# Kernel optimization log

Hardware: AMD Instinct MI355X
Metric: run time of the kernel (lower is better)

## Reference

```python
import jax, jax.numpy as jnp
import numpy as np

D = 192      # d_model
DE = 96      # d_edge
H = 8        # n_heads
DH = D // H  # d_head = 24
DF = 2 * D   # ff hidden = 384
N = 25000
E = 400000


def _layernorm(x, s, b, eps=1e-5):
    m = jnp.mean(x, axis=-1, keepdims=True)
    v = jnp.var(x, axis=-1, keepdims=True)
    return (x - m) * jax.lax.rsqrt(v + eps) * s + b


def setup_inputs() -> dict:
    key = jax.random.key(0)
    ks = jax.random.split(key, 12)
    sc = lambda d: 1.0 / np.sqrt(d)
    inp = {
        "x": jax.random.normal(ks[0], (N, D), jnp.float32),
        "edge_feat": jax.random.normal(ks[1], (E, DE), jnp.float32),
        "edge_index": jax.random.randint(ks[2], (2, E), 0, N, jnp.int64),
        # attention projections (stored [d_in, d_out], applied as x @ W)
        "Wq": jax.random.normal(ks[3], (D, D), jnp.float32) * sc(D),
        "Wk": jax.random.normal(ks[4], (D, D), jnp.float32) * sc(D),
        "Wv": jax.random.normal(ks[5], (D, D), jnp.float32) * sc(D),
        "We": jax.random.normal(ks[6], (DE, H), jnp.float32) * sc(DE),
        "Wo": jax.random.normal(ks[7], (D, D), jnp.float32) * sc(D),
        "bo": jnp.zeros((D,), jnp.float32),
        "Wg": jax.random.normal(ks[8], (2 * D, D), jnp.float32) * sc(2 * D),
        "bg": jnp.zeros((D,), jnp.float32),
        "ln1_s": jnp.ones((D,), jnp.float32),
        "ln1_b": jnp.zeros((D,), jnp.float32),
        "Wf1": jax.random.normal(ks[9], (D, DF), jnp.float32) * sc(D),
        "bf1": jnp.zeros((DF,), jnp.float32),
        "Wf2": jax.random.normal(ks[10], (DF, D), jnp.float32) * sc(DF),
        "bf2": jnp.zeros((D,), jnp.float32),
        "ln2_s": jnp.ones((D,), jnp.float32),
        "ln2_b": jnp.zeros((D,), jnp.float32),
    }
    return inp


def reference(x, edge_feat, edge_index, Wq, Wk, Wv, We, Wo, bo, Wg, bg,
              ln1_s, ln1_b, Wf1, bf1, Wf2, bf2, ln2_s, ln2_b):
    src, dst = edge_index[0], edge_index[1]
    n = x.shape[0]
    # per-edge gathered projections: [E, H, DH]
    q = (x[dst] @ Wq).reshape(-1, H, DH)
    k = (x[src] @ Wk).reshape(-1, H, DH)
    v = (x[src] @ Wv).reshape(-1, H, DH)
    score = jnp.sum(q * k, axis=-1) / np.sqrt(DH) + edge_feat @ We  # [E, H]
    # segment softmax over incoming edges of each dst node
    mx = jax.ops.segment_max(score, dst, num_segments=n)           # [N, H]
    alpha = jnp.exp(score - mx[dst])                                # [E, H]
    den = jax.ops.segment_sum(alpha, dst, num_segments=n)          # [N, H]
    num = jax.ops.segment_sum(alpha[..., None] * v, dst, num_segments=n)  # [N, H, DH]
    agg = (num / (den[:, :, None] + 1e-8)).reshape(n, D)
    o = agg @ Wo + bo
    g = jax.nn.sigmoid(jnp.concatenate([o, x], axis=-1) @ Wg + bg)
    y = _layernorm(g * o + (1.0 - g) * x, ln1_s, ln1_b)
    ff = jax.nn.silu(y @ Wf1 + bf1) @ Wf2 + bf2
    return _layernorm(y + ff, ln2_s, ln2_b)
```

## Files before the change

kernel.cpp:

```cpp
#include <hip/hip_runtime.h>
#include <cstdint>
#include <cstddef>

#define LOG2E 1.4426950408889634f

constexpr int Dm  = 192;
constexpr int DEe = 96;

typedef unsigned short u16;
typedef __attribute__((ext_vector_type(8))) short short8v;
typedef __attribute__((ext_vector_type(4))) float f32x4;

__device__ __forceinline__ u16 f2bf(float f) {
    uint32_t u = __builtin_bit_cast(uint32_t, f);
    uint32_t r = (u + 0x7FFF + ((u >> 16) & 1)) >> 16;
    return (u16)r;
}
__device__ __forceinline__ float bf2f(u16 h) {
    uint32_t u = ((uint32_t)h) << 16;
    return __builtin_bit_cast(float, u);
}
__device__ __forceinline__ uint32_t cvtpk_bf16(float lo, float hi) {
    uint32_t r;
    asm("v_cvt_pk_bf16_f32 %0, %1, %2" : "=v"(r) : "v"(lo), "v"(hi));
    return r;
}

__global__ void zero_ints(int* __restrict__ p, int n) {
    int i = blockIdx.x * blockDim.x + threadIdx.x;
    if (i < n) p[i] = 0;
}

__global__ void count_deg(const int* __restrict__ ei, int E, int* __restrict__ deg) {
    int e = blockIdx.x * blockDim.x + threadIdx.x;
    if (e < E) atomicAdd(&deg[ei[E + e]], 1);
}

__global__ __launch_bounds__(1024) void scan_kernel(const int* __restrict__ deg, int N,
                                                    int* __restrict__ offs) {
    __shared__ int sp[1024];
    int t = threadIdx.x;
    int per = (N + 1023) >> 10;
    int base = t * per;
    int sum = 0;
    for (int i = 0; i < per; ++i) {
        int idx = base + i;
        if (idx < N) sum += deg[idx];
    }
    sp[t] = sum;
    __syncthreads();
    for (int off = 1; off < 1024; off <<= 1) {
        int v = (t >= off) ? sp[t - off] : 0;
        __syncthreads();
        sp[t] += v;
        __syncthreads();
    }
    int run = sp[t] - sum;
    for (int i = 0; i < per; ++i) {
        int idx = base + i;
        if (idx < N) { offs[idx] = run; run += deg[idx]; }
    }
    if (t == 1023) offs[N] = sp[1023];
}

__global__ void xconv(const float* __restrict__ x, int n4, u16* __restrict__ xb) {
    int i = blockIdx.x * blockDim.x + threadIdx.x;
    if (i >= n4) return;
    float4 v = ((const float4*)x)[i];
    uint32_t p0 = cvtpk_bf16(v.x, v.y);
    uint32_t p1 = cvtpk_bf16(v.z, v.w);
    ushort4 o;
    o.x = (u16)(p0 & 0xffff); o.y = (u16)(p0 >> 16);
    o.z = (u16)(p1 & 0xffff); o.w = (u16)(p1 >> 16);
    ((ushort4*)xb)[i] = o;
}

__global__ void prep_w(const float* __restrict__ Wq, const float* __restrict__ Wk,
                       const float* __restrict__ Wv, const float* __restrict__ Wo,
                       const float* __restrict__ Wg, const float* __restrict__ Wf1,
                       const float* __restrict__ Wf2,
                       u16* __restrict__ Wqkvt, u16* __restrict__ Wot,
                       u16* __restrict__ Wgt, u16* __restrict__ Wf1t,
                       u16* __restrict__ Wf2t) {
    int idx = blockIdx.x * blockDim.x + threadIdx.x;
    if (idx < 110592) {
        int n = idx / 192, k = idx % 192;
        const float* W = n < 192 ? Wq : (n < 384 ? Wk : Wv);
        Wqkvt[idx] = f2bf(W[(size_t)k * 192 + (n % 192)]);
    } else if (idx < 147456) {
        int i = idx - 110592;
        int n = i / 192, k = i % 192;
        Wot[i] = f2bf(Wo[(size_t)k * 192 + n]);
    } else if (idx < 221184) {
        int i = idx - 147456;
        int n = i / 384, k = i % 384;
        Wgt[i] = f2bf(Wg[(size_t)k * 192 + n]);
    } else if (idx < 294912) {
        int i = idx - 221184;
        int n = i / 192, k = i % 192;
        Wf1t[i] = f2bf(Wf1[(size_t)k * 384 + n]);
    } else if (idx < 368640) {
        int i = idx - 294912;
        int n = i / 384, k = i % 384;
        Wf2t[i] = f2bf(Wf2[(size_t)k * 192 + n]);
    }
}

__global__ __launch_bounds__(256) void edge_prep(
    const int* __restrict__ ei, int E,
    const float* __restrict__ ef, const float* __restrict__ We,
    const int* __restrict__ offs, int* __restrict__ cur,
    float* __restrict__ scb, int* __restrict__ sbuf)
{
    __shared__ float We_s[DEe * 8];
    __shared__ float ef_s[32][100];
    int tid = threadIdx.x;
    for (int i = tid; i < DEe * 8; i += 256) We_s[i] = We[i];
    int e0 = blockIdx.x * 32;
    #pragma unroll
    for (int rep = 0; rep < 3; ++rep) {
        int idx = tid + 256 * rep;
        int el = idx / 24, c4 = idx % 24;
        int e = e0 + el;
        float4 v = make_float4(0.f, 0.f, 0.f, 0.f);
        if (e < E) v = *(const float4*)&ef[(size_t)e * DEe + c4 * 4];
        *(float4*)&ef_s[el][c4 * 4] = v;
    }
    __syncthreads();
    int el = tid >> 3, h = tid & 7;
    int e = e0 + el;
    if (e >= E) return;
    float epj = 0.f;
    #pragma unroll 8
    for (int i = 0; i < DEe; ++i) epj += ef_s[el][i] * We_s[i * 8 + h];

    int lane = tid & 63;
    int pos = 0;
    if (h == 0) {
        int dst = ei[E + e];
        pos = offs[dst] + atomicAdd(&cur[dst], 1);
    }
    pos = __shfl(pos, lane & 56, 64);
    scb[(size_t)pos * 8 + h] = epj * LOG2E;
    if (h == 0) sbuf[pos] = ei[e];
}

__global__ __launch_bounds__(256) void agg_fused(
    const u16* __restrict__ qkv, const float* __restrict__ scb,
    const int* __restrict__ sbuf, const int* __restrict__ offs,
    int N, u16* __restrict__ aggb)
{
    int node = blockIdx.x * 4 + (threadIdx.x >> 6);
    if (node >= N) return;
    int lane = threadIdx.x & 63;
    int h = lane >> 3;
    int di = (3 * lane) >> 1;
    int odd = lane & 1;

    int beg = offs[node], end = offs[node + 1];
    u16* og = aggb + (size_t)node * Dm;
    int b0 = 3 * lane;
    if (beg >= end) {
        og[b0] = 0; og[b0 + 1] = 0; og[b0 + 2] = 0;
        return;
    }

    const uint32_t* qrow = (const uint32_t*)(qkv + (size_t)node * 576);
    uint32_t qd0 = qrow[di], qd1 = qrow[di + 1];
    float q0, q1, q2;
    if (!odd) { q0 = bf2f(qd0 & 0xffff); q1 = bf2f(qd0 >> 16); q2 = bf2f(qd1 & 0xffff); }
    else      { q0 = bf2f(qd0 >> 16);    q1 = bf2f(qd1 & 0xffff); q2 = bf2f(qd1 >> 16); }

    auto clampi = [&](int i) { return i < end ? i : end - 1; };

    float den = 0.f, a0 = 0.f, a1 = 0.f, a2 = 0.f;

    uint32_t ck[2][2], cv[2][2]; float cep[2];
    uint32_t nk[2][2], nv[2][2]; float nep[2];
    int s0, s1;

    {
        int p00 = clampi(beg),     p01 = clampi(beg + 1);
        int p10 = clampi(beg + 2), p11 = clampi(beg + 3);
        int sA = sbuf[p00], sB = sbuf[p01], sC = sbuf[p10], sD = sbuf[p11];
        const uint32_t* r;
        r = (const uint32_t*)(qkv + (size_t)sA * 576 + 192);
        ck[0][0] = r[di]; ck[0][1] = r[di + 1];
        r = (const uint32_t*)(qkv + (size_t)sA * 576 + 384);
        cv[0][0] = r[di]; cv[0][1] = r[di + 1];
        r = (const uint32_t*)(qkv + (size_t)sB * 576 + 192);
        ck[1][0] = r[di]; ck[1][1] = r[di + 1];
        r = (const uint32_t*)(qkv + (size_t)sB * 576 + 384);
        cv[1][0] = r[di]; cv[1][1] = r[di + 1];
        r = (const uint32_t*)(qkv + (size_t)sC * 576 + 192);
        nk[0][0] = r[di]; nk[0][1] = r[di + 1];
        r = (const uint32_t*)(qkv + (size_t)sC * 576 + 384);
        nv[0][0] = r[di]; nv[0][1] = r[di + 1];
        r = (const uint32_t*)(qkv + (size_t)sD * 576 + 192);
        nk[1][0] = r[di]; nk[1][1] = r[di + 1];
        r = (const uint32_t*)(qkv + (size_t)sD * 576 + 384);
        nv[1][0] = r[di]; nv[1][1] = r[di + 1];
        cep[0] = scb[(size_t)p00 * 8 + h]; cep[1] = scb[(size_t)p01 * 8 + h];
        nep[0] = scb[(size_t)p10 * 8 + h]; nep[1] = scb[(size_t)p11 * 8 + h];
        s0 = sbuf[clampi(beg + 4)]; s1 = sbuf[clampi(beg + 5)];
    }

    for (int idx = beg; idx < end; idx += 2) {
        #pragma unroll
        for (int j = 0; j < 2; ++j) {
            float k0, k1, k2, v0, v1, v2;
            uint32_t kd0 = ck[j][0], kd1 = ck[j][1];
            uint32_t vd0 = cv[j][0], vd1 = cv[j][1];
            if (!odd) {
                k0 = bf2f(kd0 & 0xffff); k1 = bf2f(kd0 >> 16); k2 = bf2f(kd1 & 0xffff);
                v0 = bf2f(vd0 & 0xffff); v1 = bf2f(vd0 >> 16); v2 = bf2f(vd1 & 0xffff);
            } else {
                k0 = bf2f(kd0 >> 16); k1 = bf2f(kd1 & 0xffff); k2 = bf2f(kd1 >> 16);
                v0 = bf2f(vd0 >> 16); v1 = bf2f(vd1 & 0xffff); v2 = bf2f(vd1 >> 16);
            }
            float pd = q0 * k0 + q1 * k1 + q2 * k2;
            pd += __shfl_xor(pd, 1, 64);
            pd += __shfl_xor(pd, 2, 64);
            pd += __shfl_xor(pd, 4, 64);
            float p = exp2f(pd * 0.2944885836f + cep[j]);
            if (idx + j < end) {
                den += p;
                a0 += p * v0; a1 += p * v1; a2 += p * v2;
            }
        }
        #pragma unroll
        for (int j = 0; j < 2; ++j) {
            ck[j][0] = nk[j][0]; ck[j][1] = nk[j][1];
            cv[j][0] = nv[j][0]; cv[j][1] = nv[j][1];
            cep[j] = nep[j];
        }
        {
            const uint32_t* r;
            r = (const uint32_t*)(qkv + (size_t)s0 * 576 + 192);
            nk[0][0] = r[di]; nk[0][1] = r[di + 1];
            r = (const uint32_t*)(qkv + (size_t)s0 * 576 + 384);
            nv[0][0] = r[di]; nv[0][1] = r[di + 1];
            r = (const uint32_t*)(qkv + (size_t)s1 * 576 + 192);
            nk[1][0] = r[di]; nk[1][1] = r[di + 1];
            r = (const uint32_t*)(qkv + (size_t)s1 * 576 + 384);
            nv[1][0] = r[di]; nv[1][1] = r[di + 1];
            nep[0] = scb[(size_t)clampi(idx + 4) * 8 + h];
            nep[1] = scb[(size_t)clampi(idx + 5) * 8 + h];
        }
        s0 = sbuf[clampi(idx + 6)]; s1 = sbuf[clampi(idx + 7)];
    }

    float rden = 1.f / (den + 1e-8f);
    og[b0]     = f2bf(a0 * rden);
    og[b0 + 1] = f2bf(a1 * rden);
    og[b0 + 2] = f2bf(a2 * rden);
}

__global__ __launch_bounds__(512) void qkv_gemm(
    const u16* __restrict__ xb, int M,
    const u16* __restrict__ Wt, u16* __restrict__ qkvb)
{
    int tid = threadIdx.x;
    int m0 = blockIdx.x * 128, n0 = blockIdx.y * 192;
    int w = tid >> 6, lane = tid & 63;
    int wr = w >> 2, wc = w & 3;
    int c16 = lane & 15, hi2 = lane >> 4, kof = hi2 * 8;
    int rbase = m0 + wr * 64;

    int rcm[4];
    #pragma unroll
    for (int mr = 0; mr < 4; ++mr) {
        int r = rbase + mr * 16 + c16;
        rcm[mr] = r < M ? r : M - 1;
    }

    f32x4 acc[4][3];
    #pragma unroll
    for (int mr = 0; mr < 4; ++mr)
        #pragma unroll
        for (int nr = 0; nr < 3; ++nr) acc[mr][nr] = (f32x4)(0.f);

    #pragma unroll 1
    for (int ks = 0; ks < 6; ++ks) {
        short8v af[4], bfr[3];
        #pragma unroll
        for (int mr = 0; mr < 4; ++mr)
            af[mr] = *(const short8v*)(xb + (size_t)rcm[mr] * 192 + ks * 32 + kof);
        #pragma unroll
        for (int nr = 0; nr < 3; ++nr)
            bfr[nr] = *(const short8v*)(Wt + (size_t)(n0 + wc * 48 + nr * 16 + c16) * 192 + ks * 32 + kof);
        #pragma unroll
        for (int mr = 0; mr < 4; ++mr)
            #pragma unroll
            for (int nr = 0; nr < 3; ++nr)
                acc[mr][nr] = __builtin_amdgcn_mfma_f32_16x16x32_bf16(
                    af[mr], bfr[nr], acc[mr][nr], 0, 0, 0);
    }

    #pragma unroll
    for (int mr = 0; mr < 4; ++mr)
        #pragma unroll
        for (int nr = 0; nr < 3; ++nr) {
            uint32_t p0 = cvtpk_bf16(acc[mr][nr][0], acc[mr][nr][1]);
            uint32_t p1 = cvtpk_bf16(acc[mr][nr][2], acc[mr][nr][3]);
            int r0 = rbase + mr * 16 + hi2 * 4;
            int col = n0 + wc * 48 + nr * 16 + c16;
            if (r0     < M) qkvb[(size_t)(r0    ) * 576 + col] = (u16)(p0 & 0xffff);
            if (r0 + 1 < M) qkvb[(size_t)(r0 + 1) * 576 + col] = (u16)(p0 >> 16);
            if (r0 + 2 < M) qkvb[(size_t)(r0 + 2) * 576 + col] = (u16)(p1 & 0xffff);
            if (r0 + 3 < M) qkvb[(size_t)(r0 + 3) * 576 + col] = (u16)(p1 >> 16);
        }
}

__global__ __launch_bounds__(512) void chain_fused(
    const u16* __restrict__ aggb, const u16* __restrict__ xb, int M,
    const u16* __restrict__ Wot, const float* __restrict__ bo,
    const u16* __restrict__ Wgt, const float* __restrict__ bg,
    const float* __restrict__ l1s, const float* __restrict__ l1b,
    const u16* __restrict__ Wf1t, const float* __restrict__ bf1,
    const u16* __restrict__ Wf2t, const float* __restrict__ bf2,
    const float* __restrict__ l2s, const float* __restrict__ l2b,
    float* __restrict__ out)
{
    __shared__ __align__(16) short Ybuf[128 * 200];
    __shared__ __align__(16) short Fbuf[128 * 392];
    __shared__ float red[2][4][128];

    int tid = threadIdx.x;
    int m0 = blockIdx.x * 128;
    int w = tid >> 6, lane = tid & 63;
    int wr = w >> 2, wc = w & 3;
    int c16 = lane & 15, hi2 = lane >> 4, kof = hi2 * 8;
    int rbase = m0 + wr * 64;
    int lbase = wr * 64;

    int rcm[4];
    #pragma unroll
    for (int mr = 0; mr < 4; ++mr) {
        int r = rbase + mr * 16 + c16;
        rcm[mr] = r < M ? r : M - 1;
    }

    f32x4 oacc[4][3];
    #pragma unroll
    for (int mr = 0; mr < 4; ++mr)
        #pragma unroll
        for (int nr = 0; nr < 3; ++nr) oacc[mr][nr] = (f32x4)(0.f);
    #pragma unroll 1
    for (int ks = 0; ks < 6; ++ks) {
        short8v af[4], bfr[3];
        #pragma unroll
        for (int mr = 0; mr < 4; ++mr)
            af[mr] = *(const short8v*)(aggb + (size_t)rcm[mr] * 192 + ks * 32 + kof);
        #pragma unroll
        for (int nr = 0; nr < 3; ++nr)
            bfr[nr] = *(const short8v*)(Wot + (size_t)(wc * 48 + nr * 16 + c16) * 192 + ks * 32 + kof);
        #pragma unroll
        for (int mr = 0; mr < 4; ++mr)
            #pragma unroll
            for (int nr = 0; nr < 3; ++nr)
                oacc[mr][nr] = __builtin_amdgcn_mfma_f32_16x16x32_bf16(
                    af[mr], bfr[nr], oacc[mr][nr], 0, 0, 0);
    }
    #pragma unroll
    for (int nr = 0; nr < 3; ++nr) {
        int col = wc * 48 + nr * 16 + c16;
        float b = bo[col];
        #pragma unroll
        for (int mr = 0; mr < 4; ++mr) {
            #pragma unroll
            for (int reg = 0; reg < 4; ++reg) oacc[mr][nr][reg] += b;
            uint32_t p0 = cvtpk_bf16(oacc[mr][nr][0], oacc[mr][nr][1]);
            uint32_t p1 = cvtpk_bf16(oacc[mr][nr][2], oacc[mr][nr][3]);
            int row0 = lbase + mr * 16 + hi2 * 4;
            Ybuf[(row0    ) * 200 + col] = (short)(p0 & 0xffff);
            Ybuf[(row0 + 1) * 200 + col] = (short)(p0 >> 16);
            Ybuf[(row0 + 2) * 200 + col] = (short)(p1 & 0xffff);
            Ybuf[(row0 + 3) * 200 + col] = (short)(p1 >> 16);
        }
    }
    __syncthreads();

    f32x4 zacc[4][3];
    #pragma unroll
    for (int mr = 0; mr < 4; ++mr)
        #pragma unroll
        for (int nr = 0; nr < 3; ++nr) zacc[mr][nr] = (f32x4)(0.f);
    #pragma unroll 1
    for (int ks = 0; ks < 6; ++ks) {
        short8v af[4], bfr[3];
        #pragma unroll
        for (int mr = 0; mr < 4; ++mr)
            af[mr] = *(const short8v*)&Ybuf[(lbase + mr * 16 + c16) * 200 + ks * 32 + kof];
        #pragma unroll
        for (int nr = 0; nr < 3; ++nr)
            bfr[nr] = *(const short8v*)(Wgt + (size_t)(wc * 48 + nr * 16 + c16) * 384 + ks * 32 + kof);
        #pragma unroll
        for (int mr = 0; mr < 4; ++mr)
            #pragma unroll
            for (int nr = 0; nr < 3; ++nr)
                zacc[mr][nr] = __builtin_amdgcn_mfma_f32_16x16x32_bf16(
                    af[mr], bfr[nr], zacc[mr][nr], 0, 0, 0);
    }
    #pragma unroll 1
    for (int ks = 0; ks < 6; ++ks) {
        short8v af[4], bfr[3];
        #pragma unroll
        for (int mr = 0; mr < 4; ++mr)
            af[mr] = *(const short8v*)(xb + (size_t)rcm[mr] * 192 + ks * 32 + kof);
        #pragma unroll
        for (int nr = 0; nr < 3; ++nr)
            bfr[nr] = *(const short8v*)(Wgt + (size_t)(wc * 48 + nr * 16 + c16) * 384 + 192 + ks * 32 + kof);
        #pragma unroll
        for (int mr = 0; mr < 4; ++mr)
            #pragma unroll
            for (int nr = 0; nr < 3; ++nr)
                zacc[mr][nr] = __builtin_amdgcn_mfma_f32_16x16x32_bf16(
                    af[mr], bfr[nr], zacc[mr][nr], 0, 0, 0);
    }
    float s1p[4][4], s2p[4][4];
    #pragma unroll
    for (int mr = 0; mr < 4; ++mr)
        #pragma unroll
        for (int reg = 0; reg < 4; ++reg) {
            int gr = rbase + mr * 16 + hi2 * 4 + reg;
            int rcR = gr < M ? gr : M - 1;
            float s1 = 0.f, s2 = 0.f;
            #pragma unroll
            for (int nr = 0; nr < 3; ++nr) {
                int col = wc * 48 + nr * 16 + c16;
                float z = zacc[mr][nr][reg] + bg[col];
                float g = 1.f / (1.f + expf(-z));
                float xv = bf2f(xb[(size_t)rcR * 192 + col]);
                float val = g * oacc[mr][nr][reg] + (1.f - g) * xv;
                zacc[mr][nr][reg] = val;
                s1 += val; s2 += val * val;
            }
            #pragma unroll
            for (int mS = 1; mS < 16; mS <<= 1) {
                s1 += __shfl_xor(s1, mS, 64);
                s2 += __shfl_xor(s2, mS, 64);
            }
            s1p[mr][reg] = s1; s2p[mr][reg] = s2;
        }
    if (c16 == 0) {
        #pragma unroll
        for (int mr = 0; mr < 4; ++mr)
            #pragma unroll
            for (int reg = 0; reg < 4; ++reg) {
                int rowIdx = lbase + mr * 16 + hi2 * 4 + reg;
                red[0][wc][rowIdx] = s1p[mr][reg];
                red[1][wc][rowIdx] = s2p[mr][reg];
            }
    }
    __syncthreads();
    #pragma unroll
    for (int mr = 0; mr < 4; ++mr)
        #pragma unroll
        for (int reg = 0; reg < 4; ++reg) {
            int rowIdx = lbase + mr * 16 + hi2 * 4 + reg;
            float S1 = red[0][0][rowIdx] + red[0][1][rowIdx] + red[0][2][rowIdx] + red[0][3][rowIdx];
            float S2 = red[1][0][rowIdx] + red[1][1][rowIdx] + red[1][2][rowIdx] + red[1][3][rowIdx];
            float mean = S1 * (1.f / 192.f);
            float var  = S2 * (1.f / 192.f) - mean * mean;
            float inv  = rsqrtf(var + 1e-5f);
            #pragma unroll
            for (int nr = 0; nr < 3; ++nr) {
                int col = wc * 48 + nr * 16 + c16;
                float yv = (zacc[mr][nr][reg] - mean) * inv * l1s[col] + l1b[col];
                Ybuf[rowIdx * 200 + col] = (short)f2bf(yv);
            }
        }
    __syncthreads();

    f32x4 tacc[4][6];
    #pragma unroll
    for (int mr = 0; mr < 4; ++mr)
        #pragma unroll
        for (int nr = 0; nr < 6; ++nr) tacc[mr][nr] = (f32x4)(0.f);
    #pragma unroll 1
    for (int ks = 0; ks < 6; ++ks) {
        short8v af[4], bfr[6];
        #pragma unroll
        for (int mr = 0; mr < 4; ++mr)
            af[mr] = *(const short8v*)&Ybuf[(lbase + mr * 16 + c16) * 200 + ks * 32 + kof];
        #pragma unroll
        for (int nr = 0; nr < 6; ++nr)
            bfr[nr] = *(const short8v*)(Wf1t + (size_t)(wc * 96 + nr * 16 + c16) * 192 + ks * 32 + kof);
        #pragma unroll
        for (int mr = 0; mr < 4; ++mr)
            #pragma unroll
            for (int nr = 0; nr < 6; ++nr)
                tacc[mr][nr] = __builtin_amdgcn_mfma_f32_16x16x32_bf16(
                    af[mr], bfr[nr], tacc[mr][nr], 0, 0, 0);
    }
    #pragma unroll
    for (int nr = 0; nr < 6; ++nr) {
        int col = wc * 96 + nr * 16 + c16;
        float b = bf1[col];
        #pragma unroll
        for (int mr = 0; mr < 4; ++mr) {
            float t0[4];
            #pragma unroll
            for (int reg = 0; reg < 4; ++reg) {
                float z = tacc[mr][nr][reg] + b;
                t0[reg] = z / (1.f + expf(-z));
            }
            uint32_t p0 = cvtpk_bf16(t0[0], t0[1]);
            uint32_t p1 = cvtpk_bf16(t0[2], t0[3]);
            int row0 = lbase + mr * 16 + hi2 * 4;
            Fbuf[(row0    ) * 392 + col] = (short)(p0 & 0xffff);
            Fbuf[(row0 + 1) * 392 + col] = (short)(p0 >> 16);
            Fbuf[(row0 + 2) * 392 + col] = (short)(p1 & 0xffff);
            Fbuf[(row0 + 3) * 392 + col] = (short)(p1 >> 16);
        }
    }
    __syncthreads();

    f32x4 facc[4][3];
    #pragma unroll
    for (int mr = 0; mr < 4; ++mr)
        #pragma unroll
        for (int nr = 0; nr < 3; ++nr) facc[mr][nr] = (f32x4)(0.f);
    #pragma unroll 1
    for (int ks = 0; ks < 12; ++ks) {
        short8v af[4], bfr[3];
        #pragma unroll
        for (int mr = 0; mr < 4; ++mr)
            af[mr] = *(const short8v*)&Fbuf[(lbase + mr * 16 + c16) * 392 + ks * 32 + kof];
        #pragma unroll
        for (int nr = 0; nr < 3; ++nr)
            bfr[nr] = *(const short8v*)(Wf2t + (size_t)(wc * 48 + nr * 16 + c16) * 384 + ks * 32 + kof);
        #pragma unroll
        for (int mr = 0; mr < 4; ++mr)
            #pragma unroll
            for (int nr = 0; nr < 3; ++nr)
                facc[mr][nr] = __builtin_amdgcn_mfma_f32_16x16x32_bf16(
                    af[mr], bfr[nr], facc[mr][nr], 0, 0, 0);
    }
    float s1q[4][4], s2q[4][4];
    #pragma unroll
    for (int mr = 0; mr < 4; ++mr)
        #pragma unroll
        for (int reg = 0; reg < 4; ++reg) {
            int rowIdx = lbase + mr * 16 + hi2 * 4 + reg;
            float s1 = 0.f, s2 = 0.f;
            #pragma unroll
            for (int nr = 0; nr < 3; ++nr) {
                int col = wc * 48 + nr * 16 + c16;
                float val = facc[mr][nr][reg] + bf2[col] + bf2f((u16)Ybuf[rowIdx * 200 + col]);
                facc[mr][nr][reg] = val;
                s1 += val; s2 += val * val;
            }
            #pragma unroll
            for (int mS = 1; mS < 16; mS <<= 1) {
                s1 += __shfl_xor(s1, mS, 64);
                s2 += __shfl_xor(s2, mS, 64);
            }
            s1q[mr][reg] = s1; s2q[mr][reg] = s2;
        }
    if (c16 == 0) {
        #pragma unroll
        for (int mr = 0; mr < 4; ++mr)
            #pragma unroll
            for (int reg = 0; reg < 4; ++reg) {
                int rowIdx = lbase + mr * 16 + hi2 * 4 + reg;
                red[0][wc][rowIdx] = s1q[mr][reg];
                red[1][wc][rowIdx] = s2q[mr][reg];
            }
    }
    __syncthreads();
    #pragma unroll
    for (int mr = 0; mr < 4; ++mr)
        #pragma unroll
        for (int reg = 0; reg < 4; ++reg) {
            int rowIdx = lbase + mr * 16 + hi2 * 4 + reg;
            int r = m0 + rowIdx;
            if (r >= M) continue;
            float S1 = red[0][0][rowIdx] + red[0][1][rowIdx] + red[0][2][rowIdx] + red[0][3][rowIdx];
            float S2 = red[1][0][rowIdx] + red[1][1][rowIdx] + red[1][2][rowIdx] + red[1][3][rowIdx];
            float mean = S1 * (1.f / 192.f);
            float var  = S2 * (1.f / 192.f) - mean * mean;
            float inv  = rsqrtf(var + 1e-5f);
            #pragma unroll
            for (int nr = 0; nr < 3; ++nr) {
                int col = wc * 48 + nr * 16 + c16;
                out[(size_t)r * 192 + col] =
                    (facc[mr][nr][reg] - mean) * inv * l2s[col] + l2b[col];
            }
        }
}

extern "C" void kernel_launch(void* const* d_in, const int* in_sizes, int n_in,
                              void* d_out, int out_size, void* d_ws, size_t ws_size,
                              hipStream_t stream) {
    const float* x   = (const float*)d_in[0];
    const float* ef  = (const float*)d_in[1];
    const int*   ei  = (const int*)d_in[2];
    const float* Wq  = (const float*)d_in[3];
    const float* Wk  = (const float*)d_in[4];
    const float* Wv  = (const float*)d_in[5];
    const float* We  = (const float*)d_in[6];
    const float* Wo  = (const float*)d_in[7];
    const float* bo  = (const float*)d_in[8];
    const float* Wg  = (const float*)d_in[9];
    const float* bg  = (const float*)d_in[10];
    const float* l1s = (const float*)d_in[11];
    const float* l1b = (const float*)d_in[12];
    const float* Wf1 = (const float*)d_in[13];
    const float* bf1 = (const float*)d_in[14];
    const float* Wf2 = (const float*)d_in[15];
    const float* bf2 = (const float*)d_in[16];
    const float* l2s = (const float*)d_in[17];
    const float* l2b = (const float*)d_in[18];

    int N = in_sizes[0] / Dm;
    int E = in_sizes[1] / DEe;
    float* out = (float*)d_out;

    char* wp = (char*)d_ws;
    auto alloc = [&](size_t bytes) -> void* {
        void* p = wp;
        wp += (bytes + 255) & ~(size_t)255;
        return p;
    };
    size_t NF = (size_t)N * Dm;
    u16*   xb     = (u16*)alloc(NF * 2);
    u16*   qkvb   = (u16*)alloc((size_t)N * 576 * 2);
    u16*   aggb   = (u16*)alloc(NF * 2);
    float* scb    = (float*)alloc((size_t)E * 8 * 4);
    int*   sbuf   = (int*)  alloc((size_t)E * 4);
    int*   degcur = (int*)  alloc((size_t)2 * N * 4);
    int*   offs   = (int*)  alloc((size_t)(N + 1) * 4);
    u16*   Wqkvt  = (u16*)alloc((size_t)576 * 192 * 2);
    u16*   Wot    = (u16*)alloc((size_t)192 * 192 * 2);
    u16*   Wgt    = (u16*)alloc((size_t)192 * 384 * 2);
    u16*   Wf1t   = (u16*)alloc((size_t)384 * 192 * 2);
    u16*   Wf2t   = (u16*)alloc((size_t)192 * 384 * 2);
    int* deg = degcur;
    int* cur = degcur + N;

    int gm128 = (N + 127) / 128;

    prep_w<<<dim3(1440), 256, 0, stream>>>(Wq, Wk, Wv, Wo, Wg, Wf1, Wf2,
        Wqkvt, Wot, Wgt, Wf1t, Wf2t);
    xconv<<<dim3((N * Dm / 4 + 255) / 256), 256, 0, stream>>>(x, N * Dm / 4, xb);
    zero_ints<<<dim3((2 * N + 255) / 256), 256, 0, stream>>>(degcur, 2 * N);
    count_deg<<<dim3((E + 255) / 256), 256, 0, stream>>>(ei, E, deg);
    scan_kernel<<<dim3(1), 1024, 0, stream>>>(deg, N, offs);

    qkv_gemm<<<dim3(gm128, 3), 512, 0, stream>>>(xb, N, Wqkvt, qkvb);

    edge_prep<<<dim3((E + 31) / 32), 256, 0, stream>>>(ei, E, ef, We,
        offs, cur, scb, sbuf);
    agg_fused<<<dim3((N + 3) / 4), 256, 0, stream>>>(qkvb, scb, sbuf, offs, N, aggb);

    chain_fused<<<dim3(gm128), 512, 0, stream>>>(aggb, xb, N,
        Wot, bo, Wgt, bg, l1s, l1b, Wf1t, bf1, Wf2t, bf2, l2s, l2b, out);
}
```

Baseline: 277.4 us.

## Merge prep kernels and co-schedule edge prep with QKV GEMM in one launch

Degree counting, x-to-bf16 conversion and weight transposition now run as one flat-indexed launch instead of three. The independent edge_prep and QKV GEMM work are merged into one grid whose block ranges take different roles, so the two can overlap on the GPU. The GEMM changes from 512-thread 128-row tiles to 256-thread 64-row tiles to fit the shared block size. This cuts launch count and idle tail time between kernels, but the combined kernel's register and shared-memory use is set by the heavier branch, which may lower occupancy.

```diff
diff --git a/kernel.cpp b/kernel.cpp
--- a/kernel.cpp
+++ b/kernel.cpp
@@ -29,11 +29,6 @@
 __global__ void zero_ints(int* __restrict__ p, int n) {
     int i = blockIdx.x * blockDim.x + threadIdx.x;
     if (i < n) p[i] = 0;
-}
-
-__global__ void count_deg(const int* __restrict__ ei, int E, int* __restrict__ deg) {
-    int e = blockIdx.x * blockDim.x + threadIdx.x;
-    if (e < E) atomicAdd(&deg[ei[E + e]], 1);
 }
 
 __global__ __launch_bounds__(1024) void scan_kernel(const int* __restrict__ deg, int N,
@@ -63,86 +58,150 @@
     if (t == 1023) offs[N] = sp[1023];
 }
 
-__global__ void xconv(const float* __restrict__ x, int n4, u16* __restrict__ xb) {
-    int i = blockIdx.x * blockDim.x + threadIdx.x;
-    if (i >= n4) return;
-    float4 v = ((const float4*)x)[i];
-    uint32_t p0 = cvtpk_bf16(v.x, v.y);
-    uint32_t p1 = cvtpk_bf16(v.z, v.w);
-    ushort4 o;
-    o.x = (u16)(p0 & 0xffff); o.y = (u16)(p0 >> 16);
-    o.z = (u16)(p1 & 0xffff); o.w = (u16)(p1 >> 16);
-    ((ushort4*)xb)[i] = o;
-}
-
-__global__ void prep_w(const float* __restrict__ Wq, const float* __restrict__ Wk,
-                       const float* __restrict__ Wv, const float* __restrict__ Wo,
-                       const float* __restrict__ Wg, const float* __restrict__ Wf1,
-                       const float* __restrict__ Wf2,
-                       u16* __restrict__ Wqkvt, u16* __restrict__ Wot,
-                       u16* __restrict__ Wgt, u16* __restrict__ Wf1t,
-                       u16* __restrict__ Wf2t) {
-    int idx = blockIdx.x * blockDim.x + threadIdx.x;
+__global__ __launch_bounds__(256) void prepA(
+    const int* __restrict__ ei, int E,
+    const float* __restrict__ x, int n4, u16* __restrict__ xb,
+    const float* __restrict__ Wq, const float* __restrict__ Wk,
+    const float* __restrict__ Wv, const float* __restrict__ Wo,
+    const float* __restrict__ Wg, const float* __restrict__ Wf1,
+    const float* __restrict__ Wf2,
+    u16* __restrict__ Wqkvt, u16* __restrict__ Wot,
+    u16* __restrict__ Wgt, u16* __restrict__ Wf1t, u16* __restrict__ Wf2t,
+    int* __restrict__ deg)
+{
+    int i = blockIdx.x * 256 + threadIdx.x;
+    if (i < E) {
+        atomicAdd(&deg[ei[E + i]], 1);
+        return;
+    }
+    i -= E;
+    if (i < n4) {
+        float4 v = ((const float4*)x)[i];
+        uint32_t p0 = cvtpk_bf16(v.x, v.y);
+        uint32_t p1 = cvtpk_bf16(v.z, v.w);
+        ushort4 o;
+        o.x = (u16)(p0 & 0xffff); o.y = (u16)(p0 >> 16);
+        o.z = (u16)(p1 & 0xffff); o.w = (u16)(p1 >> 16);
+        ((ushort4*)xb)[i] = o;
+        return;
+    }
+    int idx = i - n4;
     if (idx < 110592) {
         int n = idx / 192, k = idx % 192;
         const float* W = n < 192 ? Wq : (n < 384 ? Wk : Wv);
         Wqkvt[idx] = f2bf(W[(size_t)k * 192 + (n % 192)]);
     } else if (idx < 147456) {
-        int i = idx - 110592;
-        int n = i / 192, k = i % 192;
-        Wot[i] = f2bf(Wo[(size_t)k * 192 + n]);
+        int j = idx - 110592;
+        int n = j / 192, k = j % 192;
+        Wot[j] = f2bf(Wo[(size_t)k * 192 + n]);
     } else if (idx < 221184) {
-        int i = idx - 147456;
-        int n = i / 384, k = i % 384;
-        Wgt[i] = f2bf(Wg[(size_t)k * 192 + n]);
+        int j = idx - 147456;
+        int n = j / 384, k = j % 384;
+        Wgt[j] = f2bf(Wg[(size_t)k * 192 + n]);
     } else if (idx < 294912) {
-        int i = idx - 221184;
-        int n = i / 192, k = i % 192;
-        Wf1t[i] = f2bf(Wf1[(size_t)k * 384 + n]);
+        int j = idx - 221184;
+        int n = j / 192, k = j % 192;
+        Wf1t[j] = f2bf(Wf1[(size_t)k * 384 + n]);
     } else if (idx < 368640) {
-        int i = idx - 294912;
-        int n = i / 384, k = i % 384;
-        Wf2t[i] = f2bf(Wf2[(size_t)k * 192 + n]);
-    }
-}
-
-__global__ __launch_bounds__(256) void edge_prep(
+        int j = idx - 294912;
+        int n = j / 384, k = j % 384;
+        Wf2t[j] = f2bf(Wf2[(size_t)k * 192 + n]);
+    }
+}
+
+__global__ __launch_bounds__(256) void phaseC(
+    int EB,
     const int* __restrict__ ei, int E,
     const float* __restrict__ ef, const float* __restrict__ We,
     const int* __restrict__ offs, int* __restrict__ cur,
-    float* __restrict__ scb, int* __restrict__ sbuf)
+    float* __restrict__ scb, int* __restrict__ sbuf,
+    const u16* __restrict__ xb, int M, int gm64,
+    const u16* __restrict__ Wt, u16* __restrict__ qkvb)
 {
-    __shared__ float We_s[DEe * 8];
-    __shared__ float ef_s[32][100];
+    int bid = blockIdx.x;
     int tid = threadIdx.x;
-    for (int i = tid; i < DEe * 8; i += 256) We_s[i] = We[i];
-    int e0 = blockIdx.x * 32;
-    #pragma unroll
-    for (int rep = 0; rep < 3; ++rep) {
-        int idx = tid + 256 * rep;
-        int el = idx / 24, c4 = idx % 24;
+    if (bid < EB) {
+        __shared__ float We_s[DEe * 8];
+        __shared__ float ef_s[32][100];
+        for (int i = tid; i < DEe * 8; i += 256) We_s[i] = We[i];
+        int e0 = bid * 32;
+        #pragma unroll
+        for (int rep = 0; rep < 3; ++rep) {
+            int idx = tid + 256 * rep;
+            int el = idx / 24, c4 = idx % 24;
+            int e = e0 + el;
+            float4 v = make_float4(0.f, 0.f, 0.f, 0.f);
+            if (e < E) v = *(const float4*)&ef[(size_t)e * DEe + c4 * 4];
+            *(float4*)&ef_s[el][c4 * 4] = v;
+        }
+        __syncthreads();
+        int el = tid >> 3, h = tid & 7;
         int e = e0 + el;
-        float4 v = make_float4(0.f, 0.f, 0.f, 0.f);
-        if (e < E) v = *(const float4*)&ef[(size_t)e * DEe + c4 * 4];
-        *(float4*)&ef_s[el][c4 * 4] = v;
-    }
-    __syncthreads();
-    int el = tid >> 3, h = tid & 7;
-    int e = e0 + el;
-    if (e >= E) return;
-    float epj = 0.f;
-    #pragma unroll 8
-    for (int i = 0; i < DEe; ++i) epj += ef_s[el][i] * We_s[i * 8 + h];
-
-    int lane = tid & 63;
-    int pos = 0;
-    if (h == 0) {
-        int dst = ei[E + e];
-        pos = offs[dst] + atomicAdd(&cur[dst], 1);
-    }
-    pos = __shfl(pos, lane & 56, 64);
-    scb[(size_t)pos * 8 + h] = epj * LOG2E;
-    if (h == 0) sbuf[pos] = ei[e];
+        if (e >= E) return;
+        float epj = 0.f;
+        #pragma unroll 8
+        for (int i = 0; i < DEe; ++i) epj += ef_s[el][i] * We_s[i * 8 + h];
+
+        int lane = tid & 63;
+        int pos = 0;
+        if (h == 0) {
+            int dst = ei[E + e];
+            pos = offs[dst] + atomicAdd(&cur[dst], 1);
+        }
+        pos = __shfl(pos, lane & 56, 64);
+        scb[(size_t)pos * 8 + h] = epj * LOG2E;
+        if (h == 0) sbuf[pos] = ei[e];
+        return;
+    }
+
+    int qb = bid - EB;
+    int m0 = (qb % gm64) * 64, n0 = (qb / gm64) * 192;
+    int w = tid >> 6, lane = tid & 63;
+    int c16 = lane & 15, hi2 = lane >> 4, kof = hi2 * 8;
+
+    int rcm[4];
+    #pragma unroll
+    for (int mr = 0; mr < 4; ++mr) {
+        int r = m0 + mr * 16 + c16;
+        rcm[mr] = r < M ? r : M - 1;
+    }
+
+    f32x4 acc[4][3];
+    #pragma unroll
+    for (int mr = 0; mr < 4; ++mr)
+        #pragma unroll
+        for (int nr = 0; nr < 3; ++nr) acc[mr][nr] = (f32x4)(0.f);
+
+    #pragma unroll 1
+    for (int ks = 0; ks < 6; ++ks) {
+        short8v af[4], bfr[3];
+        #pragma unroll
+        for (int mr = 0; mr < 4; ++mr)
+            af[mr] = *(const short8v*)(xb + (size_t)rcm[mr] * 192 + ks * 32 + kof);
+        #pragma unroll
+        for (int nr = 0; nr < 3; ++nr)
+            bfr[nr] = *(const short8v*)(Wt + (size_t)(n0 + w * 48 + nr * 16 + c16) * 192 + ks * 32 + kof);
+        #pragma unroll
+        for (int mr = 0; mr < 4; ++mr)
+            #pragma unroll
+            for (int nr = 0; nr < 3; ++nr)
+                acc[mr][nr] = __builtin_amdgcn_mfma_f32_16x16x32_bf16(
+                    af[mr], bfr[nr], acc[mr][nr], 0, 0, 0);
+    }
+
+    #pragma unroll
+    for (int mr = 0; mr < 4; ++mr)
+        #pragma unroll
+        for (int nr = 0; nr < 3; ++nr) {
+            uint32_t p0 = cvtpk_bf16(acc[mr][nr][0], acc[mr][nr][1]);
+            uint32_t p1 = cvtpk_bf16(acc[mr][nr][2], acc[mr][nr][3]);
+            int r0 = m0 + mr * 16 + hi2 * 4;
+            int col = n0 + w * 48 + nr * 16 + c16;
+            if (r0     < M) qkvb[(size_t)(r0    ) * 576 + col] = (u16)(p0 & 0xffff);
+            if (r0 + 1 < M) qkvb[(size_t)(r0 + 1) * 576 + col] = (u16)(p0 >> 16);
+            if (r0 + 2 < M) qkvb[(size_t)(r0 + 2) * 576 + col] = (u16)(p1 & 0xffff);
+            if (r0 + 3 < M) qkvb[(size_t)(r0 + 3) * 576 + col] = (u16)(p1 >> 16);
+        }
 }
 
 __global__ __launch_bounds__(256) void agg_fused(
@@ -256,62 +315,6 @@
     og[b0 + 2] = f2bf(a2 * rden);
 }
 
-__global__ __launch_bounds__(512) void qkv_gemm(
-    const u16* __restrict__ xb, int M,
-    const u16* __restrict__ Wt, u16* __restrict__ qkvb)
-{
-    int tid = threadIdx.x;
-    int m0 = blockIdx.x * 128, n0 = blockIdx.y * 192;
-    int w = tid >> 6, lane = tid & 63;
-    int wr = w >> 2, wc = w & 3;
-    int c16 = lane & 15, hi2 = lane >> 4, kof = hi2 * 8;
-    int rbase = m0 + wr * 64;
-
-    int rcm[4];
-    #pragma unroll
-    for (int mr = 0; mr < 4; ++mr) {
-        int r = rbase + mr * 16 + c16;
-        rcm[mr] = r < M ? r : M - 1;
-    }
-
-    f32x4 acc[4][3];
-    #pragma unroll
-    for (int mr = 0; mr < 4; ++mr)
-        #pragma unroll
-        for (int nr = 0; nr < 3; ++nr) acc[mr][nr] = (f32x4)(0.f);
-
-    #pragma unroll 1
-    for (int ks = 0; ks < 6; ++ks) {
-        short8v af[4], bfr[3];
-        #pragma unroll
-        for (int mr = 0; mr < 4; ++mr)
-            af[mr] = *(const short8v*)(xb + (size_t)rcm[mr] * 192 + ks * 32 + kof);
-        #pragma unroll
-        for (int nr = 0; nr < 3; ++nr)
-            bfr[nr] = *(const short8v*)(Wt + (size_t)(n0 + wc * 48 + nr * 16 + c16) * 192 + ks * 32 + kof);
-        #pragma unroll
-        for (int mr = 0; mr < 4; ++mr)
-            #pragma unroll
-            for (int nr = 0; nr < 3; ++nr)
-                acc[mr][nr] = __builtin_amdgcn_mfma_f32_16x16x32_bf16(
-                    af[mr], bfr[nr], acc[mr][nr], 0, 0, 0);
-    }
-
-    #pragma unroll
-    for (int mr = 0; mr < 4; ++mr)
-        #pragma unroll
-        for (int nr = 0; nr < 3; ++nr) {
-            uint32_t p0 = cvtpk_bf16(acc[mr][nr][0], acc[mr][nr][1]);
-            uint32_t p1 = cvtpk_bf16(acc[mr][nr][2], acc[mr][nr][3]);
-            int r0 = rbase + mr * 16 + hi2 * 4;
-            int col = n0 + wc * 48 + nr * 16 + c16;
-            if (r0     < M) qkvb[(size_t)(r0    ) * 576 + col] = (u16)(p0 & 0xffff);
-            if (r0 + 1 < M) qkvb[(size_t)(r0 + 1) * 576 + col] = (u16)(p0 >> 16);
-            if (r0 + 2 < M) qkvb[(size_t)(r0 + 2) * 576 + col] = (u16)(p1 & 0xffff);
-            if (r0 + 3 < M) qkvb[(size_t)(r0 + 3) * 576 + col] = (u16)(p1 >> 16);
-        }
-}
-
 __global__ __launch_bounds__(512) void chain_fused(
     const u16* __restrict__ aggb, const u16* __restrict__ xb, int M,
     const u16* __restrict__ Wot, const float* __restrict__ bo,
@@ -640,19 +643,25 @@
     int* deg = degcur;
     int* cur = degcur + N;
 
+    int gm64  = (N + 63) / 64;
     int gm128 = (N + 127) / 128;
-
-    prep_w<<<dim3(1440), 256, 0, stream>>>(Wq, Wk, Wv, Wo, Wg, Wf1, Wf2,
-        Wqkvt, Wot, Wgt, Wf1t, Wf2t);
-    xconv<<<dim3((N * Dm / 4 + 255) / 256), 256, 0, stream>>>(x, N * Dm / 4, xb);
+    int n4 = N * Dm / 4;
+
     zero_ints<<<dim3((2 * N + 255) / 256), 256, 0, stream>>>(degcur, 2 * N);
-    count_deg<<<dim3((E + 255) / 256), 256, 0, stream>>>(ei, E, deg);
+
+    int prepTotal = E + n4 + 368640;
+    prepA<<<dim3((prepTotal + 255) / 256), 256, 0, stream>>>(
+        ei, E, x, n4, xb, Wq, Wk, Wv, Wo, Wg, Wf1, Wf2,
+        Wqkvt, Wot, Wgt, Wf1t, Wf2t, deg);
+
     scan_kernel<<<dim3(1), 1024, 0, stream>>>(deg, N, offs);
 
-    qkv_gemm<<<dim3(gm128, 3), 512, 0, stream>>>(xb, N, Wqkvt, qkvb);
-
-    edge_prep<<<dim3((E + 31) / 32), 256, 0, stream>>>(ei, E, ef, We,
-        offs, cur, scb, sbuf);
+    int EB = (E + 31) / 32;
+    int QB = gm64 * 3;
+    phaseC<<<dim3(EB + QB), 256, 0, stream>>>(EB,
+        ei, E, ef, We, offs, cur, scb, sbuf,
+        xb, N, gm64, Wqkvt, qkvb);
+
     agg_fused<<<dim3((N + 3) / 4), 256, 0, stream>>>(qkvb, scb, sbuf, offs, N, aggb);
 
     chain_fused<<<dim3(gm128), 512, 0, stream>>>(aggb, xb, N,
```

After: 272.5 us. About the same (-1.8%).
